# Kernel optimization log

Measured on AMD Instinct MI355X. Metric: run time of the kernel, lower is better.

## Reference

```python
import jax, jax.numpy as jnp
import numpy as np

N, E, G = 50000, 800000, 256
H, C = 8, 16
F0 = 64
FH = H * C  # 128
L = 6
EPS = 1e-5
SEL = [0, 1, 2, 3, 4, 5, 5, 5]  # <10 layers -> pad with last


def setup_inputs() -> dict:
    key = jax.random.key(0)
    ks = jax.random.split(key, 32)

    def w(k, shape, fan_in):
        return jax.random.normal(k, shape, jnp.float32) / np.float32(np.sqrt(fan_in))

    inp = {
        'x': jax.random.normal(ks[0], (N, F0), jnp.float32),
        'edge_index': jax.random.randint(ks[1], (2, E), 0, N),
        'batch_vec': jnp.sort(jax.random.randint(ks[2], (N,), 0, G)),
        # layer 0 (in=F0)
        'Wq0': w(ks[3], (F0, FH), F0), 'bq0': 0.01 * jax.random.normal(ks[4], (FH,), jnp.float32),
        'Wk0': w(ks[5], (F0, FH), F0), 'bk0': 0.01 * jax.random.normal(ks[6], (FH,), jnp.float32),
        'Wv0': w(ks[7], (F0, FH), F0), 'bv0': 0.01 * jax.random.normal(ks[8], (FH,), jnp.float32),
        'Ws0': w(ks[9], (F0, FH), F0), 'bs0': 0.01 * jax.random.normal(ks[10], (FH,), jnp.float32),
        # layers 1..L-1 (in=FH), stacked
        'Wq': w(ks[11], (L - 1, FH, FH), FH), 'bq': 0.01 * jax.random.normal(ks[12], (L - 1, FH), jnp.float32),
        'Wk': w(ks[13], (L - 1, FH, FH), FH), 'bk': 0.01 * jax.random.normal(ks[14], (L - 1, FH), jnp.float32),
        'Wv': w(ks[15], (L - 1, FH, FH), FH), 'bv': 0.01 * jax.random.normal(ks[16], (L - 1, FH), jnp.float32),
        'Ws': w(ks[17], (L - 1, FH, FH), FH), 'bs': 0.01 * jax.random.normal(ks[18], (L - 1, FH), jnp.float32),
        # BatchNorm affine params per layer
        'gamma': jnp.ones((L, FH), jnp.float32),
        'beta': jnp.zeros((L, FH), jnp.float32),
    }
    return inp


def _transformer_conv(x, src, dst, Wq, bq, Wk, bk, Wv, bv, Ws, bs):
    # q from target nodes, k/v from source nodes (PyG TransformerConv, concat=True)
    q = (x @ Wq + bq).reshape(-1, H, C)
    k = (x @ Wk + bk).reshape(-1, H, C)
    v = (x @ Wv + bv).reshape(-1, H, C)
    s = jnp.einsum('ehc,ehc->eh', q[dst], k[src]) * np.float32(1.0 / np.sqrt(C))  # [E,H]
    m = jax.ops.segment_max(s, dst, num_segments=N)       # segment softmax over in-edges
    e = jnp.exp(s - m[dst])
    denom = jax.ops.segment_sum(e, dst, num_segments=N)
    alpha = e / jnp.maximum(denom[dst], 1e-16)            # [E,H]
    msg = jax.ops.segment_sum(alpha[:, :, None] * v[src], dst, num_segments=N)  # [N,H,C]
    return msg.reshape(-1, FH) + (x @ Ws + bs)            # root/skip connection


def _bn_relu(x, g, b):
    mu = jnp.mean(x, axis=0)
    var = jnp.var(x, axis=0)  # biased, as used for normalization in training mode
    return jax.nn.relu((x - mu) * jax.lax.rsqrt(var + EPS) * g + b)


def reference(x, edge_index, batch_vec, Wq0, bq0, Wk0, bk0, Wv0, bv0, Ws0, bs0,
              Wq, bq, Wk, bk, Wv, bv, Ws, bs, gamma, beta):
    src, dst = edge_index[0], edge_index[1]
    outs = []
    h = _bn_relu(_transformer_conv(x, src, dst, Wq0, bq0, Wk0, bk0, Wv0, bv0, Ws0, bs0),
                 gamma[0], beta[0])
    outs.append(h)
    for i in range(L - 1):
        h = _bn_relu(_transformer_conv(h, src, dst, Wq[i], bq[i], Wk[i], bk[i],
                                       Wv[i], bv[i], Ws[i], bs[i]),
                     gamma[i + 1], beta[i + 1])
        outs.append(h)
    counts = jnp.maximum(jax.ops.segment_sum(jnp.ones((N,), x.dtype), batch_vec, num_segments=G), 1.0)
    pooled = [jax.ops.segment_sum(o, batch_vec, num_segments=G) / counts[:, None] for o in outs]
    latent = jnp.stack([pooled[i] for i in SEL], axis=1)  # [G, 8, FH]
    return latent.reshape(G, -1)                          # [G, 8*FH]
```

## Files before the change

kernel.cpp:

```cpp
#include <hip/hip_runtime.h>
#include <hip/hip_bf16.h>
#include <math.h>

#define NN 50000
#define NE 800000
#define NG 256
#define FHH 128
#define NL 6
#define NCH 49
#define NB 391

typedef __attribute__((ext_vector_type(8))) short s16x8;
typedef __attribute__((ext_vector_type(4))) float f32x4;

#define QSCALE 0.36067376022224085f

#if defined(__has_builtin)
#if __has_builtin(__builtin_amdgcn_fdot2_f32_bf16)
#define HAVE_BFDOT 1
#endif
#endif
#ifndef HAVE_BFDOT
#define HAVE_BFDOT 0
#endif

__device__ __forceinline__ ushort f2bf(float x) {
  uint u = __float_as_uint(x);
  u += 0x7fffu + ((u >> 16) & 1u);
  return (ushort)(u >> 16);
}
__device__ __forceinline__ float bf2f(ushort h) {
  return __uint_as_float(((uint)h) << 16);
}
__device__ __forceinline__ float bfl(uint u) { return __uint_as_float(u << 16); }
__device__ __forceinline__ float bfh(uint u) { return __uint_as_float(u & 0xffff0000u); }
__device__ __forceinline__ uint packbf(float a, float b) {
  return (uint)f2bf(a) | ((uint)f2bf(b) << 16);
}

#if HAVE_BFDOT
typedef __attribute__((ext_vector_type(2))) __bf16 bf16v2;
__device__ __forceinline__ float dot2acc(uint a, uint b, float acc) {
  return __builtin_amdgcn_fdot2_f32_bf16(__builtin_bit_cast(bf16v2, a),
                                         __builtin_bit_cast(bf16v2, b), acc, false);
}
#endif

__device__ __forceinline__ void gload16(const ushort* g, ushort* l) {
  __builtin_amdgcn_global_load_lds(
      (const __attribute__((address_space(1))) uint*)(const void*)g,
      (__attribute__((address_space(3))) uint*)(void*)l, 16, 0, 0);
}

__global__ void k_gstart(const int* __restrict__ bv, int* __restrict__ gstart) {
  int g = blockIdx.x * blockDim.x + threadIdx.x;
  if (g > NG) return;
  int lo = 0, hi = NN;
  while (lo < hi) { int mid = (lo + hi) >> 1; if (bv[mid] < g) lo = mid + 1; else hi = mid; }
  gstart[g] = lo;
}

__global__ void k_deg(const int* __restrict__ dstv, int* __restrict__ deg) {
  int e = blockIdx.x * blockDim.x + threadIdx.x;
  if (e < NE) atomicAdd(&deg[dstv[e]], 1);
}

__global__ __launch_bounds__(256) void k_scanA(const int* __restrict__ deg, int* __restrict__ part) {
  int b = blockIdx.x, t = threadIdx.x;
  int s = 0;
  for (int j = t; j < 1024; j += 256) { int i = b * 1024 + j; if (i < NN) s += deg[i]; }
  __shared__ int sh[4];
  for (int o = 32; o; o >>= 1) s += __shfl_down(s, o, 64);
  if ((t & 63) == 0) sh[t >> 6] = s;
  __syncthreads();
  if (t == 0) part[b] = sh[0] + sh[1] + sh[2] + sh[3];
}

__global__ void k_scanB(int* __restrict__ part, int* __restrict__ row_ptr) {
  if (threadIdx.x == 0 && blockIdx.x == 0) {
    int run = 0;
    for (int i = 0; i < NCH; ++i) { int v = part[i]; part[i] = run; run += v; }
    row_ptr[NN] = run;
  }
}

__global__ __launch_bounds__(1024) void k_scanC(const int* __restrict__ deg, const int* __restrict__ part,
                                                int* __restrict__ row_ptr, int* __restrict__ cursor) {
  __shared__ int buf[1024];
  int b = blockIdx.x, t = threadIdx.x;
  int i = b * 1024 + t;
  int v = (i < NN) ? deg[i] : 0;
  buf[t] = v;
  __syncthreads();
  for (int off = 1; off < 1024; off <<= 1) {
    int add = (t >= off) ? buf[t - off] : 0;
    __syncthreads();
    buf[t] += add;
    __syncthreads();
  }
  if (i < NN) { int ex = part[b] + buf[t] - v; row_ptr[i] = ex; cursor[i] = ex; }
}

__global__ void k_scatter(const int* __restrict__ srcv, const int* __restrict__ dstv,
                          int* __restrict__ cursor, uint* __restrict__ colb) {
  int e = blockIdx.x * blockDim.x + threadIdx.x;
  if (e < NE) {
    int d = dstv[e];
    int pos = atomicAdd(&cursor[d], 1);
    colb[pos] = ((uint)srcv[e]) << 9;
  }
}

__device__ __forceinline__ size_t wtile_idx(int k, int c) {
  return (size_t)(k >> 5) * 4096 + ((((c >> 4) * 4 + ((k & 31) >> 3)) * 16 + (c & 15)) * 8 + (k & 7));
}

__global__ __launch_bounds__(256) void k_wconv0(const float* __restrict__ W0, const float* __restrict__ W1,
                                                const float* __restrict__ W2, const float* __restrict__ W3,
                                                ushort* __restrict__ wh, ushort* __restrict__ wl) {
  int id = blockIdx.x * 256 + threadIdx.x;
  if (id >= 4 * 64 * 128) return;
  int mat = id >> 13, rem = id & 8191;
  int k = rem >> 7, c = rem & 127;
  const float* W = (mat == 0) ? W0 : (mat == 1) ? W1 : (mat == 2) ? W2 : W3;
  float v = W[k * 128 + c];
  ushort h = f2bf(v);
  ushort lo = f2bf(v - bf2f(h));
  size_t dst = (size_t)mat * 8192 + wtile_idx(k, c);
  wh[dst] = h; wl[dst] = lo;
}

__global__ __launch_bounds__(256) void k_wconvS(const float* __restrict__ Wq, const float* __restrict__ Wk,
                                                const float* __restrict__ Wv, const float* __restrict__ Ws,
                                                ushort* __restrict__ wh, ushort* __restrict__ wl) {
  int id = blockIdx.x * 256 + threadIdx.x;
  if (id >= 5 * 4 * 16384) return;
  int lay = id / 65536, rem = id % 65536;
  int mat = rem >> 14, rem2 = rem & 16383;
  int k = rem2 >> 7, c = rem2 & 127;
  const float* W = (mat == 0) ? Wq : (mat == 1) ? Wk : (mat == 2) ? Wv : Ws;
  float v = W[(size_t)lay * 16384 + k * 128 + c];
  ushort h = f2bf(v);
  ushort lo = f2bf(v - bf2f(h));
  size_t dst = 32768 + ((size_t)lay * 4 + mat) * 16384 + wtile_idx(k, c);
  wh[dst] = h; wl[dst] = lo;
}

template <int K>
__global__ __launch_bounds__(256) void k_presplit(const float* __restrict__ Y,
                                                  ushort* __restrict__ Xh) {
  const int CP = K / 4;
  int idx = blockIdx.x * 256 + threadIdx.x;
  int row = idx / CP;
  int c4 = (idx % CP) * 4;
  if (row >= NN) return;
  float4 v = *reinterpret_cast<const float4*>(Y + (size_t)row * K + c4);
  ushort h0 = f2bf(v.x), h1 = f2bf(v.y), h2 = f2bf(v.z), h3 = f2bf(v.w);
  int b = row >> 7, g = (row & 127) >> 4, frow = row & 15;
  int ks = c4 >> 5, qq = (c4 & 31) >> 3, j = c4 & 7;
  size_t base = ((size_t)ks * NB + b) * 4096 + (((g * 4 + qq) * 16) + frow) * 8 + j;
  *reinterpret_cast<uint2*>(Xh + base) =
      make_uint2((uint)h0 | ((uint)h1 << 16), (uint)h2 | ((uint)h3 << 16));
}

template <int K>
__global__ __launch_bounds__(256, 3) void k_gemm(
    const ushort* __restrict__ Xh,
    const ushort* __restrict__ Wth, const ushort* __restrict__ Wtl,
    const float* __restrict__ b0, const float* __restrict__ b1,
    const float* __restrict__ b2, const float* __restrict__ b3,
    ushort* __restrict__ qbf, ushort* __restrict__ kv, ushort* __restrict__ xsb) {
  __shared__ __align__(16) ushort Ah[4096];
  __shared__ __align__(16) ushort Bh[4096];
  __shared__ __align__(16) ushort Bl[4096];
  int bid = blockIdx.x;
  int mat = (bid >> 3) & 3;
  int b = (bid & 7) + ((bid >> 5) << 3);
  if (b >= NB) return;
  int t = threadIdx.x;
  int lane = t & 63, w = t >> 6;
  int wr = w >> 1, wc = w & 1;
  int frow = lane & 15;
  const ushort* wh = Wth + (size_t)mat * (K * 128);
  const ushort* wl = Wtl + (size_t)mat * (K * 128);
  const float* bb = (mat == 0) ? b0 : (mat == 1) ? b1 : (mat == 2) ? b2 : b3;

  f32x4 acc[4][4];
#pragma unroll
  for (int i = 0; i < 4; ++i)
#pragma unroll
    for (int j = 0; j < 4; ++j)
#pragma unroll
      for (int r = 0; r < 4; ++r) acc[i][j][r] = 0.f;

  int wofs = w * 1024 + lane * 8;
  for (int ks = 0; ks < K / 32; ++ks) {
    size_t abase = ((size_t)ks * NB + b) * 4096;
    const ushort* gAh = Xh + abase + wofs;
    const ushort* gBh = wh + ks * 4096 + wofs;
    const ushort* gBl = wl + ks * 4096 + wofs;
    gload16(gAh, &Ah[w * 1024]);
    gload16(gAh + 512, &Ah[w * 1024 + 512]);
    gload16(gBh, &Bh[w * 1024]);
    gload16(gBh + 512, &Bh[w * 1024 + 512]);
    gload16(gBl, &Bl[w * 1024]);
    gload16(gBl + 512, &Bl[w * 1024 + 512]);
    __syncthreads();
    s16x8 ah[4], bh[4], bl[4];
#pragma unroll
    for (int g = 0; g < 4; ++g) {
      ah[g] = *reinterpret_cast<const s16x8*>(&Ah[(wr * 4 + g) * 512 + lane * 8]);
      bh[g] = *reinterpret_cast<const s16x8*>(&Bh[(wc * 4 + g) * 512 + lane * 8]);
      bl[g] = *reinterpret_cast<const s16x8*>(&Bl[(wc * 4 + g) * 512 + lane * 8]);
    }
#pragma unroll
    for (int rg = 0; rg < 4; ++rg)
#pragma unroll
      for (int cg = 0; cg < 4; ++cg) {
        acc[rg][cg] = __builtin_amdgcn_mfma_f32_16x16x32_bf16(ah[rg], bh[cg], acc[rg][cg], 0, 0, 0);
        acc[rg][cg] = __builtin_amdgcn_mfma_f32_16x16x32_bf16(ah[rg], bl[cg], acc[rg][cg], 0, 0, 0);
      }
    __syncthreads();
  }
  int r0 = b * 128;
  int qq = (lane >> 4) << 2;
#pragma unroll
  for (int rg = 0; rg < 4; ++rg) {
#pragma unroll
    for (int cg = 0; cg < 4; ++cg) {
      int colg = wc * 64 + cg * 16 + frow;
      float bv = bb[colg];
#pragma unroll
      for (int r = 0; r < 4; ++r) {
        int row = r0 + wr * 64 + rg * 16 + qq + r;
        if (row >= NN) continue;
        float val = acc[rg][cg][r] + bv;
        if (mat == 0)      qbf[(size_t)row * FHH + colg] = f2bf(val * QSCALE);
        else if (mat == 3) xsb[(size_t)row * FHH + colg] = f2bf(val);
        else {
          int pos = (colg >> 1) * 4 + ((mat == 2) ? 2 : 0) + (colg & 1);
          kv[(size_t)row * 256 + pos] = f2bf(val);
        }
      }
    }
  }
}

__global__ __launch_bounds__(256) void k_agg(const uint* __restrict__ qb,
                                             const ushort* __restrict__ kv,
                                             const uint* __restrict__ xsb,
                                             const int* __restrict__ row_ptr,
                                             const uint* __restrict__ colb,
                                             uint* __restrict__ yb) {
  int n = blockIdx.x * 4 + (threadIdx.x >> 6);
  int lane = threadIdx.x & 63;
  int hl = lane & 31, half = lane >> 5;
  uint2 qp = *reinterpret_cast<const uint2*>(qb + (n << 6) + 2 * hl);
#if !HAVE_BFDOT
  float qa = bfl(qp.x), qbv = bfh(qp.x), qc = bfl(qp.y), qd = bfh(qp.y);
#endif
  const char* kvb = (const char*)kv;
  uint tof = (uint)hl * 16u;
  int e0 = row_ptr[n], e1 = row_ptr[n + 1];
  float sum = 0.f, a0 = 0.f, a1 = 0.f, a2 = 0.f, a3 = 0.f;
  int i = e0;
#define QKDOT(d, p)                                                    \
  {                                                                    \
    p = qa * bfl(d.x);                                                 \
    p = fmaf(qbv, bfh(d.x), p);                                        \
    p = fmaf(qc, bfl(d.z), p);                                         \
    p = fmaf(qd, bfh(d.z), p);                                         \
  }
  for (; i + 8 <= e1; i += 8) {
    uint oA = colb[i + half] + tof;
    uint oB = colb[i + 2 + half] + tof;
    uint oC = colb[i + 4 + half] + tof;
    uint oD = colb[i + 6 + half] + tof;
    uint4 dA = *(const uint4*)(kvb + oA);
    uint4 dB = *(const uint4*)(kvb + oB);
    uint4 dC = *(const uint4*)(kvb + oC);
    uint4 dD = *(const uint4*)(kvb + oD);
    float pA, pB, pC, pD;
#if HAVE_BFDOT
    pA = dot2acc(dA.z, qp.y, dot2acc(dA.x, qp.x, 0.f));
    pB = dot2acc(dB.z, qp.y, dot2acc(dB.x, qp.x, 0.f));
    pC = dot2acc(dC.z, qp.y, dot2acc(dC.x, qp.x, 0.f));
    pD = dot2acc(dD.z, qp.y, dot2acc(dD.x, qp.x, 0.f));
#else
    QKDOT(dA, pA) QKDOT(dB, pB) QKDOT(dC, pC) QKDOT(dD, pD)
#endif
    pA += __shfl_xor(pA, 1, 4);  pB += __shfl_xor(pB, 1, 4);
    pC += __shfl_xor(pC, 1, 4);  pD += __shfl_xor(pD, 1, 4);
    pA += __shfl_xor(pA, 2, 4);  pB += __shfl_xor(pB, 2, 4);
    pC += __shfl_xor(pC, 2, 4);  pD += __shfl_xor(pD, 2, 4);
    float wA = exp2f(fminf(pA, 110.f));
    float wB = exp2f(fminf(pB, 110.f));
    float wC = exp2f(fminf(pC, 110.f));
    float wD = exp2f(fminf(pD, 110.f));
    sum += (wA + wB) + (wC + wD);
    a0 = fmaf(wA, bfl(dA.y), fmaf(wB, bfl(dB.y), fmaf(wC, bfl(dC.y), fmaf(wD, bfl(dD.y), a0))));
    a1 = fmaf(wA, bfh(dA.y), fmaf(wB, bfh(dB.y), fmaf(wC, bfh(dC.y), fmaf(wD, bfh(dD.y), a1))));
    a2 = fmaf(wA, bfl(dA.w), fmaf(wB, bfl(dB.w), fmaf(wC, bfl(dC.w), fmaf(wD, bfl(dD.w), a2))));
    a3 = fmaf(wA, bfh(dA.w), fmaf(wB, bfh(dB.w), fmaf(wC, bfh(dC.w), fmaf(wD, bfh(dD.w), a3))));
  }
  for (; i + 2 <= e1; i += 2) {
    uint oA = colb[i + half] + tof;
    uint4 dA = *(const uint4*)(kvb + oA);
    float pA;
#if HAVE_BFDOT
    pA = dot2acc(dA.z, qp.y, dot2acc(dA.x, qp.x, 0.f));
#else
    QKDOT(dA, pA)
#endif
    pA += __shfl_xor(pA, 1, 4);
    pA += __shfl_xor(pA, 2, 4);
    float wA = exp2f(fminf(pA, 110.f));
    sum += wA;
    a0 = fmaf(wA, bfl(dA.y), a0);
    a1 = fmaf(wA, bfh(dA.y), a1);
    a2 = fmaf(wA, bfl(dA.w), a2);
    a3 = fmaf(wA, bfh(dA.w), a3);
  }
  if (i < e1) {
    uint oA = colb[i] + tof;
    uint4 dA = *(const uint4*)(kvb + oA);
    float pA;
#if HAVE_BFDOT
    pA = dot2acc(dA.z, qp.y, dot2acc(dA.x, qp.x, 0.f));
#else
    QKDOT(dA, pA)
#endif
    pA += __shfl_xor(pA, 1, 4);
    pA += __shfl_xor(pA, 2, 4);
    float wA = exp2f(fminf(pA, 110.f));
    if (half) wA = 0.f;
    sum += wA;
    a0 = fmaf(wA, bfl(dA.y), a0);
    a1 = fmaf(wA, bfh(dA.y), a1);
    a2 = fmaf(wA, bfl(dA.w), a2);
    a3 = fmaf(wA, bfh(dA.w), a3);
  }
#undef QKDOT
  sum += __shfl_xor(sum, 32);
  a0 += __shfl_xor(a0, 32);
  a1 += __shfl_xor(a1, 32);
  a2 += __shfl_xor(a2, 32);
  a3 += __shfl_xor(a3, 32);
  float inv = 1.f / fmaxf(sum, 1e-16f);
  uint2 xv = *reinterpret_cast<const uint2*>(xsb + (n << 6) + 2 * hl);
  float o0 = fmaf(a0, inv, bfl(xv.x));
  float o1 = fmaf(a1, inv, bfh(xv.x));
  float o2 = fmaf(a2, inv, bfl(xv.y));
  float o3 = fmaf(a3, inv, bfh(xv.y));
  if (half == 0) {
    uint2 o;
    o.x = packbf(o0, o1);
    o.y = packbf(o2, o3);
    *reinterpret_cast<uint2*>(yb + (n << 6) + 2 * hl) = o;
  }
}

__global__ __launch_bounds__(256) void k_bnstats(const uint* __restrict__ yb,
                                                 float* __restrict__ stats) {
  __shared__ float2 s1[256], s2[256];
  int u = threadIdx.x & 63;
  int grp = threadIdx.x >> 6;
  float2 a = make_float2(0.f, 0.f), b = make_float2(0.f, 0.f);
  for (int r = blockIdx.x * 4 + grp; r < NN; r += 1024) {
    uint d = yb[(size_t)r * 64 + u];
    float x = bfl(d), yv = bfh(d);
    a.x += x; a.y += yv;
    b.x = fmaf(x, x, b.x); b.y = fmaf(yv, yv, b.y);
  }
  s1[threadIdx.x] = a;
  s2[threadIdx.x] = b;
  __syncthreads();
  if (grp == 0) {
#pragma unroll
    for (int g = 1; g < 4; ++g) {
      a.x += s1[u + 64 * g].x; a.y += s1[u + 64 * g].y;
      b.x += s2[u + 64 * g].x; b.y += s2[u + 64 * g].y;
    }
    atomicAdd(&stats[2 * u], a.x);
    atomicAdd(&stats[2 * u + 1], a.y);
    atomicAdd(&stats[128 + 2 * u], b.x);
    atomicAdd(&stats[128 + 2 * u + 1], b.y);
  }
}

template <int WRITE_X>
__global__ __launch_bounds__(256) void k_post(const uint* __restrict__ yb,
                                              const float* __restrict__ st,
                                              const float* __restrict__ gvec,
                                              const float* __restrict__ bvec_,
                                              const int* __restrict__ bv,
                                              const int* __restrict__ gstart,
                                              float* __restrict__ out, int layer,
                                              ushort* __restrict__ Xh) {
  __shared__ float acts[8][128];
  __shared__ int sg[8];
  __shared__ float ssc[128], ssh[128];
  int b = blockIdx.x, t = threadIdx.x;
  if (t < 128) {
    const float invn = 1.f / (float)NN;
    float mu = st[t] * invn;
    float var = st[128 + t] * invn - mu * mu;
    float sc = gvec[t] * rsqrtf(var + 1e-5f);
    ssc[t] = sc;
    ssh[t] = bvec_[t] - mu * sc;
  }
  if (t < 8) sg[t] = (b * 8 + t < NN) ? bv[b * 8 + t] : -1;
  __syncthreads();
  int row = b * 8 + (t >> 5);
  int c4 = (t & 31) * 4;
  bool ok = row < NN;
  float4 a = make_float4(0.f, 0.f, 0.f, 0.f);
  if (ok) {
    uint2 u2 = *reinterpret_cast<const uint2*>(yb + (size_t)row * 64 + (c4 >> 1));
    a.x = fmaxf(fmaf(bfl(u2.x), ssc[c4 + 0], ssh[c4 + 0]), 0.f);
    a.y = fmaxf(fmaf(bfh(u2.x), ssc[c4 + 1], ssh[c4 + 1]), 0.f);
    a.z = fmaxf(fmaf(bfl(u2.y), ssc[c4 + 2], ssh[c4 + 2]), 0.f);
    a.w = fmaxf(fmaf(bfh(u2.y), ssc[c4 + 3], ssh[c4 + 3]), 0.f);
  }
  *reinterpret_cast<float4*>(&acts[t >> 5][c4]) = a;
  if (WRITE_X && ok) {
    ushort h0 = f2bf(a.x), h1 = f2bf(a.y), h2 = f2bf(a.z), h3 = f2bf(a.w);
    int bb = row >> 7, g = (row & 127) >> 4, frow = row & 15;
    int ks = c4 >> 5, qq = (c4 & 31) >> 3, j = c4 & 7;
    size_t base = ((size_t)ks * NB + bb) * 4096 + (((g * 4 + qq) * 16) + frow) * 8 + j;
    *reinterpret_cast<uint2*>(Xh + base) =
        make_uint2((uint)h0 | ((uint)h1 << 16), (uint)h2 | ((uint)h3 << 16));
  }
  __syncthreads();
  if (t < 128) {
    float racc = 0.f;
    int cg = sg[0];
    for (int r = 0; r < 8; ++r) {
      int g = sg[r];
      if (g != cg) {
        if (cg >= 0) {
          float p = racc / (float)(gstart[cg + 1] - gstart[cg]);
          if (layer < 5) atomicAdd(&out[(size_t)cg * 1024 + layer * FHH + t], p);
          else {
            atomicAdd(&out[(size_t)cg * 1024 + 5 * FHH + t], p);
            atomicAdd(&out[(size_t)cg * 1024 + 6 * FHH + t], p);
            atomicAdd(&out[(size_t)cg * 1024 + 7 * FHH + t], p);
          }
        }
        racc = 0.f;
        cg = g;
      }
      racc += acts[r][t];
    }
    if (cg >= 0) {
      float p = racc / (float)(gstart[cg + 1] - gstart[cg]);
      if (layer < 5) atomicAdd(&out[(size_t)cg * 1024 + layer * FHH + t], p);
      else {
        atomicAdd(&out[(size_t)cg * 1024 + 5 * FHH + t], p);
        atomicAdd(&out[(size_t)cg * 1024 + 6 * FHH + t], p);
        atomicAdd(&out[(size_t)cg * 1024 + 7 * FHH + t], p);
      }
    }
  }
}

extern "C" void kernel_launch(void* const* d_in, const int* in_sizes, int n_in,
                              void* d_out, int out_size, void* d_ws, size_t ws_size,
                              hipStream_t stream) {
  (void)in_sizes; (void)n_in; (void)ws_size;
  const float* x    = (const float*)d_in[0];
  const int*   ei   = (const int*)d_in[1];
  const int*   bvec = (const int*)d_in[2];
  const float* Wq0  = (const float*)d_in[3];
  const float* bq0  = (const float*)d_in[4];
  const float* Wk0  = (const float*)d_in[5];
  const float* bk0  = (const float*)d_in[6];
  const float* Wv0  = (const float*)d_in[7];
  const float* bv0  = (const float*)d_in[8];
  const float* Ws0  = (const float*)d_in[9];
  const float* bs0  = (const float*)d_in[10];
  const float* WqS  = (const float*)d_in[11];
  const float* bqS  = (const float*)d_in[12];
  const float* WkS  = (const float*)d_in[13];
  const float* bkS  = (const float*)d_in[14];
  const float* WvS  = (const float*)d_in[15];
  const float* bvS  = (const float*)d_in[16];
  const float* WsS  = (const float*)d_in[17];
  const float* bsS  = (const float*)d_in[18];
  const float* gamma = (const float*)d_in[19];
  const float* beta  = (const float*)d_in[20];
  float* out = (float*)d_out;

  char* ws = (char*)d_ws;
  size_t off = 0;
  auto alloc = [&](size_t bytes) {
    void* p = ws + off;
    off = (off + bytes + 255) & ~(size_t)255;
    return p;
  };
  ushort* qbf = (ushort*)alloc((size_t)NN * FHH * 2);
  ushort* xsb = (ushort*)alloc((size_t)NN * FHH * 2);
  uint* yb    = (uint*)alloc((size_t)NN * 64 * 4);
  ushort* kv  = (ushort*)alloc((size_t)NN * 256 * 2);
  ushort* Xh  = (ushort*)alloc((size_t)4 * NB * 4096 * 2 + 8192);
  uint* colb   = (uint*)alloc((size_t)NE * 4);
  int* row_ptr = (int*)alloc((size_t)(NN + 1) * 4);
  int* cursor  = (int*)alloc((size_t)NN * 4);
  int* deg     = (int*)alloc((size_t)NN * 4);
  int* part    = (int*)alloc((size_t)NCH * 4);
  int* gstart  = (int*)alloc((size_t)(NG + 1) * 4);
  float* bstat = (float*)alloc((size_t)NL * 2 * FHH * 4);
  ushort* wsh = (ushort*)alloc((size_t)360448 * 2);
  ushort* wsl = (ushort*)alloc((size_t)360448 * 2);

  const int* srcv = ei;
  const int* dstv = ei + NE;

  hipMemsetAsync(out, 0, (size_t)out_size * 4, stream);
  hipMemsetAsync(deg, 0, (size_t)NN * 4, stream);
  hipMemsetAsync(bstat, 0, (size_t)NL * 2 * FHH * 4, stream);
  k_gstart<<<5, 64, 0, stream>>>(bvec, gstart);
  k_deg<<<(NE + 255) / 256, 256, 0, stream>>>(dstv, deg);
  k_scanA<<<NCH, 256, 0, stream>>>(deg, part);
  k_scanB<<<1, 64, 0, stream>>>(part, row_ptr);
  k_scanC<<<NCH, 1024, 0, stream>>>(deg, part, row_ptr, cursor);
  k_scatter<<<(NE + 255) / 256, 256, 0, stream>>>(srcv, dstv, cursor, colb);
  k_wconv0<<<128, 256, 0, stream>>>(Wq0, Wk0, Wv0, Ws0, wsh, wsl);
  k_wconvS<<<1280, 256, 0, stream>>>(WqS, WkS, WvS, WsS, wsh, wsl);
  k_presplit<64><<<(NN * 16 + 255) / 256, 256, 0, stream>>>(x, Xh);

  const int GEMM_GRID = 49 * 32;
  for (int l = 0; l < NL; ++l) {
    const ushort* WthL = wsh + ((l == 0) ? 0 : (size_t)32768 + (size_t)(l - 1) * 65536);
    const ushort* WtlL = wsl + ((l == 0) ? 0 : (size_t)32768 + (size_t)(l - 1) * 65536);
    const float *bq_, *bk_, *bv_, *bs_;
    if (l == 0) { bq_ = bq0; bk_ = bk0; bv_ = bv0; bs_ = bs0; }
    else {
      size_t bo = (size_t)(l - 1) * FHH;
      bq_ = bqS + bo; bk_ = bkS + bo; bv_ = bvS + bo; bs_ = bsS + bo;
    }
    if (l == 0)
      k_gemm<64><<<GEMM_GRID, 256, 0, stream>>>(Xh, WthL, WtlL, bq_, bk_, bv_, bs_, qbf, kv, xsb);
    else
      k_gemm<128><<<GEMM_GRID, 256, 0, stream>>>(Xh, WthL, WtlL, bq_, bk_, bv_, bs_, qbf, kv, xsb);
    k_agg<<<NN / 4, 256, 0, stream>>>((const uint*)qbf, kv, (const uint*)xsb, row_ptr, colb, yb);
    float* lstat = bstat + (size_t)l * 2 * FHH;
    k_bnstats<<<256, 256, 0, stream>>>(yb, lstat);
    if (l + 1 < NL)
      k_post<1><<<6250, 256, 0, stream>>>(yb, lstat, gamma + (size_t)l * FHH,
                                          beta + (size_t)l * FHH, bvec, gstart, out, l, Xh);
    else
      k_post<0><<<6250, 256, 0, stream>>>(yb, lstat, gamma + (size_t)l * FHH,
                                          beta + (size_t)l * FHH, bvec, gstart, out, l, Xh);
  }
}
```

Baseline: 901.3 us.

## Fuse all layer kernels into one persistent cooperative kernel with grid syncs

Replaces the 24 per-layer launches (gemm, agg, bnstats, post) with a single cooperative persistent kernel that loops over layers and phases, separated by grid-wide syncs. Blocks walk tiles and nodes with grid-stride loops, sized from the occupancy query. The aim is to remove launch overhead and inter-kernel gaps. The cost is grid.sync overhead, lower occupancy from one shared register and LDS budget across all phases, and loss of the bf16 dot2 path in the aggregation.

```diff
diff --git a/kernel.cpp b/kernel.cpp
--- a/kernel.cpp
+++ b/kernel.cpp
@@ -1,6 +1,9 @@
 #include <hip/hip_runtime.h>
 #include <hip/hip_bf16.h>
+#include <hip/hip_cooperative_groups.h>
 #include <math.h>
+
+namespace cg = cooperative_groups;
 
 #define NN 50000
 #define NE 800000
@@ -9,20 +12,12 @@
 #define NL 6
 #define NCH 49
 #define NB 391
+#define NTILE (49 * 32)
 
 typedef __attribute__((ext_vector_type(8))) short s16x8;
 typedef __attribute__((ext_vector_type(4))) float f32x4;
 
 #define QSCALE 0.36067376022224085f
-
-#if defined(__has_builtin)
-#if __has_builtin(__builtin_amdgcn_fdot2_f32_bf16)
-#define HAVE_BFDOT 1
-#endif
-#endif
-#ifndef HAVE_BFDOT
-#define HAVE_BFDOT 0
-#endif
 
 __device__ __forceinline__ ushort f2bf(float x) {
   uint u = __float_as_uint(x);
@@ -37,14 +32,6 @@
 __device__ __forceinline__ uint packbf(float a, float b) {
   return (uint)f2bf(a) | ((uint)f2bf(b) << 16);
 }
-
-#if HAVE_BFDOT
-typedef __attribute__((ext_vector_type(2))) __bf16 bf16v2;
-__device__ __forceinline__ float dot2acc(uint a, uint b, float acc) {
-  return __builtin_amdgcn_fdot2_f32_bf16(__builtin_bit_cast(bf16v2, a),
-                                         __builtin_bit_cast(bf16v2, b), acc, false);
-}
-#endif
 
 __device__ __forceinline__ void gload16(const ushort* g, ushort* l) {
   __builtin_amdgcn_global_load_lds(
@@ -163,304 +150,316 @@
       make_uint2((uint)h0 | ((uint)h1 << 16), (uint)h2 | ((uint)h3 << 16));
 }
 
-template <int K>
-__global__ __launch_bounds__(256, 3) void k_gemm(
-    const ushort* __restrict__ Xh,
-    const ushort* __restrict__ Wth, const ushort* __restrict__ Wtl,
-    const float* __restrict__ b0, const float* __restrict__ b1,
-    const float* __restrict__ b2, const float* __restrict__ b3,
-    ushort* __restrict__ qbf, ushort* __restrict__ kv, ushort* __restrict__ xsb) {
-  __shared__ __align__(16) ushort Ah[4096];
-  __shared__ __align__(16) ushort Bh[4096];
-  __shared__ __align__(16) ushort Bl[4096];
-  int bid = blockIdx.x;
-  int mat = (bid >> 3) & 3;
-  int b = (bid & 7) + ((bid >> 5) << 3);
-  if (b >= NB) return;
-  int t = threadIdx.x;
-  int lane = t & 63, w = t >> 6;
-  int wr = w >> 1, wc = w & 1;
-  int frow = lane & 15;
-  const ushort* wh = Wth + (size_t)mat * (K * 128);
-  const ushort* wl = Wtl + (size_t)mat * (K * 128);
-  const float* bb = (mat == 0) ? b0 : (mat == 1) ? b1 : (mat == 2) ? b2 : b3;
-
-  f32x4 acc[4][4];
-#pragma unroll
-  for (int i = 0; i < 4; ++i)
-#pragma unroll
-    for (int j = 0; j < 4; ++j)
-#pragma unroll
-      for (int r = 0; r < 4; ++r) acc[i][j][r] = 0.f;
-
-  int wofs = w * 1024 + lane * 8;
-  for (int ks = 0; ks < K / 32; ++ks) {
-    size_t abase = ((size_t)ks * NB + b) * 4096;
-    const ushort* gAh = Xh + abase + wofs;
-    const ushort* gBh = wh + ks * 4096 + wofs;
-    const ushort* gBl = wl + ks * 4096 + wofs;
-    gload16(gAh, &Ah[w * 1024]);
-    gload16(gAh + 512, &Ah[w * 1024 + 512]);
-    gload16(gBh, &Bh[w * 1024]);
-    gload16(gBh + 512, &Bh[w * 1024 + 512]);
-    gload16(gBl, &Bl[w * 1024]);
-    gload16(gBl + 512, &Bl[w * 1024 + 512]);
-    __syncthreads();
-    s16x8 ah[4], bh[4], bl[4];
-#pragma unroll
-    for (int g = 0; g < 4; ++g) {
-      ah[g] = *reinterpret_cast<const s16x8*>(&Ah[(wr * 4 + g) * 512 + lane * 8]);
-      bh[g] = *reinterpret_cast<const s16x8*>(&Bh[(wc * 4 + g) * 512 + lane * 8]);
-      bl[g] = *reinterpret_cast<const s16x8*>(&Bl[(wc * 4 + g) * 512 + lane * 8]);
+__global__ __launch_bounds__(256) void k_layers(
+    const ushort* __restrict__ wsh, const ushort* __restrict__ wsl,
+    const float* __restrict__ bq0, const float* __restrict__ bk0,
+    const float* __restrict__ bv0, const float* __restrict__ bs0,
+    const float* __restrict__ bqS, const float* __restrict__ bkS,
+    const float* __restrict__ bvS, const float* __restrict__ bsS,
+    const float* __restrict__ gamma, const float* __restrict__ beta,
+    const int* __restrict__ bvec, const int* __restrict__ gstart,
+    const int* __restrict__ row_ptr, const uint* __restrict__ colb,
+    ushort* __restrict__ qbf, ushort* __restrict__ kv, ushort* __restrict__ xsb,
+    uint* __restrict__ yb, ushort* __restrict__ Xh,
+    float* __restrict__ bstat, float* __restrict__ out) {
+  cg::grid_group grid = cg::this_grid();
+  __shared__ __align__(16) char sbuf[24576];
+  ushort* Ah = (ushort*)sbuf;
+  ushort* Bh = (ushort*)(sbuf + 8192);
+  ushort* Bl = (ushort*)(sbuf + 16384);
+  const int NBLK = gridDim.x;
+  const int t = threadIdx.x;
+
+  for (int l = 0; l < NL; ++l) {
+    const int K = (l == 0) ? 64 : 128;
+    const int nks = K >> 5;
+    const int matstride = K << 7;
+    const ushort* WthL = wsh + ((l == 0) ? 0 : (size_t)32768 + (size_t)(l - 1) * 65536);
+    const ushort* WtlL = wsl + ((l == 0) ? 0 : (size_t)32768 + (size_t)(l - 1) * 65536);
+    const float *bq_, *bk_, *bv_, *bs_;
+    if (l == 0) { bq_ = bq0; bk_ = bk0; bv_ = bv0; bs_ = bs0; }
+    else {
+      size_t bo = (size_t)(l - 1) * FHH;
+      bq_ = bqS + bo; bk_ = bkS + bo; bv_ = bvS + bo; bs_ = bsS + bo;
     }
-#pragma unroll
-    for (int rg = 0; rg < 4; ++rg)
-#pragma unroll
-      for (int cg = 0; cg < 4; ++cg) {
-        acc[rg][cg] = __builtin_amdgcn_mfma_f32_16x16x32_bf16(ah[rg], bh[cg], acc[rg][cg], 0, 0, 0);
-        acc[rg][cg] = __builtin_amdgcn_mfma_f32_16x16x32_bf16(ah[rg], bl[cg], acc[rg][cg], 0, 0, 0);
-      }
-    __syncthreads();
-  }
-  int r0 = b * 128;
-  int qq = (lane >> 4) << 2;
-#pragma unroll
-  for (int rg = 0; rg < 4; ++rg) {
-#pragma unroll
-    for (int cg = 0; cg < 4; ++cg) {
-      int colg = wc * 64 + cg * 16 + frow;
-      float bv = bb[colg];
-#pragma unroll
-      for (int r = 0; r < 4; ++r) {
-        int row = r0 + wr * 64 + rg * 16 + qq + r;
-        if (row >= NN) continue;
-        float val = acc[rg][cg][r] + bv;
-        if (mat == 0)      qbf[(size_t)row * FHH + colg] = f2bf(val * QSCALE);
-        else if (mat == 3) xsb[(size_t)row * FHH + colg] = f2bf(val);
-        else {
-          int pos = (colg >> 1) * 4 + ((mat == 2) ? 2 : 0) + (colg & 1);
-          kv[(size_t)row * 256 + pos] = f2bf(val);
-        }
+    float* lstat = bstat + (size_t)l * 2 * FHH;
+
+    {
+      int lane = t & 63, w = t >> 6;
+      int wr = w >> 1, wc = w & 1;
+      int frow = lane & 15;
+      int wofs = w * 1024 + lane * 8;
+      for (int tile = blockIdx.x; tile < NTILE; tile += NBLK) {
+        int mat = (tile >> 3) & 3;
+        int b = (tile & 7) + ((tile >> 5) << 3);
+        if (b < NB) {
+          const ushort* wh = WthL + (size_t)mat * matstride;
+          const ushort* wl = WtlL + (size_t)mat * matstride;
+          const float* bb = (mat == 0) ? bq_ : (mat == 1) ? bk_ : (mat == 2) ? bv_ : bs_;
+          f32x4 acc[4][4];
+#pragma unroll
+          for (int i = 0; i < 4; ++i)
+#pragma unroll
+            for (int j = 0; j < 4; ++j)
+#pragma unroll
+              for (int r = 0; r < 4; ++r) acc[i][j][r] = 0.f;
+          for (int ks = 0; ks < nks; ++ks) {
+            size_t abase = ((size_t)ks * NB + b) * 4096;
+            const ushort* gAh = Xh + abase + wofs;
+            const ushort* gBh = wh + ks * 4096 + wofs;
+            const ushort* gBl = wl + ks * 4096 + wofs;
+            gload16(gAh, &Ah[w * 1024]);
+            gload16(gAh + 512, &Ah[w * 1024 + 512]);
+            gload16(gBh, &Bh[w * 1024]);
+            gload16(gBh + 512, &Bh[w * 1024 + 512]);
+            gload16(gBl, &Bl[w * 1024]);
+            gload16(gBl + 512, &Bl[w * 1024 + 512]);
+            __syncthreads();
+            s16x8 ah[4], bh[4], bl[4];
+#pragma unroll
+            for (int g = 0; g < 4; ++g) {
+              ah[g] = *reinterpret_cast<const s16x8*>(&Ah[(wr * 4 + g) * 512 + lane * 8]);
+              bh[g] = *reinterpret_cast<const s16x8*>(&Bh[(wc * 4 + g) * 512 + lane * 8]);
+              bl[g] = *reinterpret_cast<const s16x8*>(&Bl[(wc * 4 + g) * 512 + lane * 8]);
+            }
+#pragma unroll
+            for (int rg = 0; rg < 4; ++rg)
+#pragma unroll
+              for (int cg2 = 0; cg2 < 4; ++cg2) {
+                acc[rg][cg2] = __builtin_amdgcn_mfma_f32_16x16x32_bf16(ah[rg], bh[cg2], acc[rg][cg2], 0, 0, 0);
+                acc[rg][cg2] = __builtin_amdgcn_mfma_f32_16x16x32_bf16(ah[rg], bl[cg2], acc[rg][cg2], 0, 0, 0);
+              }
+            __syncthreads();
+          }
+          int r0 = b * 128;
+          int qq = (lane >> 4) << 2;
+#pragma unroll
+          for (int rg = 0; rg < 4; ++rg) {
+#pragma unroll
+            for (int cg2 = 0; cg2 < 4; ++cg2) {
+              int colg = wc * 64 + cg2 * 16 + frow;
+              float bv = bb[colg];
+#pragma unroll
+              for (int r = 0; r < 4; ++r) {
+                int row = r0 + wr * 64 + rg * 16 + qq + r;
+                if (row >= NN) continue;
+                float val = acc[rg][cg2][r] + bv;
+                if (mat == 0)      qbf[(size_t)row * FHH + colg] = f2bf(val * QSCALE);
+                else if (mat == 3) xsb[(size_t)row * FHH + colg] = f2bf(val);
+                else {
+                  int pos = (colg >> 1) * 4 + ((mat == 2) ? 2 : 0) + (colg & 1);
+                  kv[(size_t)row * 256 + pos] = f2bf(val);
+                }
+              }
+            }
+          }
+        }
+        __syncthreads();
       }
     }
-  }
-}
-
-__global__ __launch_bounds__(256) void k_agg(const uint* __restrict__ qb,
-                                             const ushort* __restrict__ kv,
-                                             const uint* __restrict__ xsb,
-                                             const int* __restrict__ row_ptr,
-                                             const uint* __restrict__ colb,
-                                             uint* __restrict__ yb) {
-  int n = blockIdx.x * 4 + (threadIdx.x >> 6);
-  int lane = threadIdx.x & 63;
-  int hl = lane & 31, half = lane >> 5;
-  uint2 qp = *reinterpret_cast<const uint2*>(qb + (n << 6) + 2 * hl);
-#if !HAVE_BFDOT
-  float qa = bfl(qp.x), qbv = bfh(qp.x), qc = bfl(qp.y), qd = bfh(qp.y);
-#endif
-  const char* kvb = (const char*)kv;
-  uint tof = (uint)hl * 16u;
-  int e0 = row_ptr[n], e1 = row_ptr[n + 1];
-  float sum = 0.f, a0 = 0.f, a1 = 0.f, a2 = 0.f, a3 = 0.f;
-  int i = e0;
-#define QKDOT(d, p)                                                    \
-  {                                                                    \
-    p = qa * bfl(d.x);                                                 \
-    p = fmaf(qbv, bfh(d.x), p);                                        \
-    p = fmaf(qc, bfl(d.z), p);                                         \
-    p = fmaf(qd, bfh(d.z), p);                                         \
-  }
-  for (; i + 8 <= e1; i += 8) {
-    uint oA = colb[i + half] + tof;
-    uint oB = colb[i + 2 + half] + tof;
-    uint oC = colb[i + 4 + half] + tof;
-    uint oD = colb[i + 6 + half] + tof;
-    uint4 dA = *(const uint4*)(kvb + oA);
-    uint4 dB = *(const uint4*)(kvb + oB);
-    uint4 dC = *(const uint4*)(kvb + oC);
-    uint4 dD = *(const uint4*)(kvb + oD);
-    float pA, pB, pC, pD;
-#if HAVE_BFDOT
-    pA = dot2acc(dA.z, qp.y, dot2acc(dA.x, qp.x, 0.f));
-    pB = dot2acc(dB.z, qp.y, dot2acc(dB.x, qp.x, 0.f));
-    pC = dot2acc(dC.z, qp.y, dot2acc(dC.x, qp.x, 0.f));
-    pD = dot2acc(dD.z, qp.y, dot2acc(dD.x, qp.x, 0.f));
-#else
-    QKDOT(dA, pA) QKDOT(dB, pB) QKDOT(dC, pC) QKDOT(dD, pD)
-#endif
-    pA += __shfl_xor(pA, 1, 4);  pB += __shfl_xor(pB, 1, 4);
-    pC += __shfl_xor(pC, 1, 4);  pD += __shfl_xor(pD, 1, 4);
-    pA += __shfl_xor(pA, 2, 4);  pB += __shfl_xor(pB, 2, 4);
-    pC += __shfl_xor(pC, 2, 4);  pD += __shfl_xor(pD, 2, 4);
-    float wA = exp2f(fminf(pA, 110.f));
-    float wB = exp2f(fminf(pB, 110.f));
-    float wC = exp2f(fminf(pC, 110.f));
-    float wD = exp2f(fminf(pD, 110.f));
-    sum += (wA + wB) + (wC + wD);
-    a0 = fmaf(wA, bfl(dA.y), fmaf(wB, bfl(dB.y), fmaf(wC, bfl(dC.y), fmaf(wD, bfl(dD.y), a0))));
-    a1 = fmaf(wA, bfh(dA.y), fmaf(wB, bfh(dB.y), fmaf(wC, bfh(dC.y), fmaf(wD, bfh(dD.y), a1))));
-    a2 = fmaf(wA, bfl(dA.w), fmaf(wB, bfl(dB.w), fmaf(wC, bfl(dC.w), fmaf(wD, bfl(dD.w), a2))));
-    a3 = fmaf(wA, bfh(dA.w), fmaf(wB, bfh(dB.w), fmaf(wC, bfh(dC.w), fmaf(wD, bfh(dD.w), a3))));
-  }
-  for (; i + 2 <= e1; i += 2) {
-    uint oA = colb[i + half] + tof;
-    uint4 dA = *(const uint4*)(kvb + oA);
-    float pA;
-#if HAVE_BFDOT
-    pA = dot2acc(dA.z, qp.y, dot2acc(dA.x, qp.x, 0.f));
-#else
-    QKDOT(dA, pA)
-#endif
-    pA += __shfl_xor(pA, 1, 4);
-    pA += __shfl_xor(pA, 2, 4);
-    float wA = exp2f(fminf(pA, 110.f));
-    sum += wA;
-    a0 = fmaf(wA, bfl(dA.y), a0);
-    a1 = fmaf(wA, bfh(dA.y), a1);
-    a2 = fmaf(wA, bfl(dA.w), a2);
-    a3 = fmaf(wA, bfh(dA.w), a3);
-  }
-  if (i < e1) {
-    uint oA = colb[i] + tof;
-    uint4 dA = *(const uint4*)(kvb + oA);
-    float pA;
-#if HAVE_BFDOT
-    pA = dot2acc(dA.z, qp.y, dot2acc(dA.x, qp.x, 0.f));
-#else
-    QKDOT(dA, pA)
-#endif
-    pA += __shfl_xor(pA, 1, 4);
-    pA += __shfl_xor(pA, 2, 4);
-    float wA = exp2f(fminf(pA, 110.f));
-    if (half) wA = 0.f;
-    sum += wA;
-    a0 = fmaf(wA, bfl(dA.y), a0);
-    a1 = fmaf(wA, bfh(dA.y), a1);
-    a2 = fmaf(wA, bfl(dA.w), a2);
-    a3 = fmaf(wA, bfh(dA.w), a3);
-  }
+    grid.sync();
+
+    {
+      const uint* qb = (const uint*)qbf;
+      const uint* xsu = (const uint*)xsb;
+      const char* kvb = (const char*)kv;
+      int lane = t & 63;
+      int hl = lane & 31, half = lane >> 5;
+      uint tof = (uint)hl * 16u;
+      for (int nb = blockIdx.x; nb < NN / 4; nb += NBLK) {
+        int n = nb * 4 + (t >> 6);
+        uint2 qp = *reinterpret_cast<const uint2*>(qb + (n << 6) + 2 * hl);
+        float qa = bfl(qp.x), qbv = bfh(qp.x), qc = bfl(qp.y), qd = bfh(qp.y);
+        int e0 = row_ptr[n], e1 = row_ptr[n + 1];
+        float sum = 0.f, a0 = 0.f, a1 = 0.f, a2 = 0.f, a3 = 0.f;
+        int i = e0;
+#define QKDOT(d, p)                                                  \
+        {                                                            \
+          p = qa * bfl(d.x);                                         \
+          p = fmaf(qbv, bfh(d.x), p);                                \
+          p = fmaf(qc, bfl(d.z), p);                                 \
+          p = fmaf(qd, bfh(d.z), p);                                 \
+        }
+        for (; i + 8 <= e1; i += 8) {
+          uint oA = colb[i + half] + tof;
+          uint oB = colb[i + 2 + half] + tof;
+          uint oC = colb[i + 4 + half] + tof;
+          uint oD = colb[i + 6 + half] + tof;
+          uint4 dA = *(const uint4*)(kvb + oA);
+          uint4 dB = *(const uint4*)(kvb + oB);
+          uint4 dC = *(const uint4*)(kvb + oC);
+          uint4 dD = *(const uint4*)(kvb + oD);
+          float pA, pB, pC, pD;
+          QKDOT(dA, pA) QKDOT(dB, pB) QKDOT(dC, pC) QKDOT(dD, pD)
+          pA += __shfl_xor(pA, 1, 4);  pB += __shfl_xor(pB, 1, 4);
+          pC += __shfl_xor(pC, 1, 4);  pD += __shfl_xor(pD, 1, 4);
+          pA += __shfl_xor(pA, 2, 4);  pB += __shfl_xor(pB, 2, 4);
+          pC += __shfl_xor(pC, 2, 4);  pD += __shfl_xor(pD, 2, 4);
+          float wA = exp2f(fminf(pA, 110.f));
+          float wB = exp2f(fminf(pB, 110.f));
+          float wC = exp2f(fminf(pC, 110.f));
+          float wD = exp2f(fminf(pD, 110.f));
+          sum += (wA + wB) + (wC + wD);
+          a0 = fmaf(wA, bfl(dA.y), fmaf(wB, bfl(dB.y), fmaf(wC, bfl(dC.y), fmaf(wD, bfl(dD.y), a0))));
+          a1 = fmaf(wA, bfh(dA.y), fmaf(wB, bfh(dB.y), fmaf(wC, bfh(dC.y), fmaf(wD, bfh(dD.y), a1))));
+          a2 = fmaf(wA, bfl(dA.w), fmaf(wB, bfl(dB.w), fmaf(wC, bfl(dC.w), fmaf(wD, bfl(dD.w), a2))));
+          a3 = fmaf(wA, bfh(dA.w), fmaf(wB, bfh(dB.w), fmaf(wC, bfh(dC.w), fmaf(wD, bfh(dD.w), a3))));
+        }
+        for (; i + 2 <= e1; i += 2) {
+          uint oA = colb[i + half] + tof;
+          uint4 dA = *(const uint4*)(kvb + oA);
+          float pA;
+          QKDOT(dA, pA)
+          pA += __shfl_xor(pA, 1, 4);
+          pA += __shfl_xor(pA, 2, 4);
+          float wA = exp2f(fminf(pA, 110.f));
+          sum += wA;
+          a0 = fmaf(wA, bfl(dA.y), a0);
+          a1 = fmaf(wA, bfh(dA.y), a1);
+          a2 = fmaf(wA, bfl(dA.w), a2);
+          a3 = fmaf(wA, bfh(dA.w), a3);
+        }
+        if (i < e1) {
+          uint oA = colb[i] + tof;
+          uint4 dA = *(const uint4*)(kvb + oA);
+          float pA;
+          QKDOT(dA, pA)
+          pA += __shfl_xor(pA, 1, 4);
+          pA += __shfl_xor(pA, 2, 4);
+          float wA = exp2f(fminf(pA, 110.f));
+          if (half) wA = 0.f;
+          sum += wA;
+          a0 = fmaf(wA, bfl(dA.y), a0);
+          a1 = fmaf(wA, bfh(dA.y), a1);
+          a2 = fmaf(wA, bfl(dA.w), a2);
+          a3 = fmaf(wA, bfh(dA.w), a3);
+        }
 #undef QKDOT
-  sum += __shfl_xor(sum, 32);
-  a0 += __shfl_xor(a0, 32);
-  a1 += __shfl_xor(a1, 32);
-  a2 += __shfl_xor(a2, 32);
-  a3 += __shfl_xor(a3, 32);
-  float inv = 1.f / fmaxf(sum, 1e-16f);
-  uint2 xv = *reinterpret_cast<const uint2*>(xsb + (n << 6) + 2 * hl);
-  float o0 = fmaf(a0, inv, bfl(xv.x));
-  float o1 = fmaf(a1, inv, bfh(xv.x));
-  float o2 = fmaf(a2, inv, bfl(xv.y));
-  float o3 = fmaf(a3, inv, bfh(xv.y));
-  if (half == 0) {
-    uint2 o;
-    o.x = packbf(o0, o1);
-    o.y = packbf(o2, o3);
-    *reinterpret_cast<uint2*>(yb + (n << 6) + 2 * hl) = o;
-  }
-}
-
-__global__ __launch_bounds__(256) void k_bnstats(const uint* __restrict__ yb,
-                                                 float* __restrict__ stats) {
-  __shared__ float2 s1[256], s2[256];
-  int u = threadIdx.x & 63;
-  int grp = threadIdx.x >> 6;
-  float2 a = make_float2(0.f, 0.f), b = make_float2(0.f, 0.f);
-  for (int r = blockIdx.x * 4 + grp; r < NN; r += 1024) {
-    uint d = yb[(size_t)r * 64 + u];
-    float x = bfl(d), yv = bfh(d);
-    a.x += x; a.y += yv;
-    b.x = fmaf(x, x, b.x); b.y = fmaf(yv, yv, b.y);
-  }
-  s1[threadIdx.x] = a;
-  s2[threadIdx.x] = b;
-  __syncthreads();
-  if (grp == 0) {
-#pragma unroll
-    for (int g = 1; g < 4; ++g) {
-      a.x += s1[u + 64 * g].x; a.y += s1[u + 64 * g].y;
-      b.x += s2[u + 64 * g].x; b.y += s2[u + 64 * g].y;
-    }
-    atomicAdd(&stats[2 * u], a.x);
-    atomicAdd(&stats[2 * u + 1], a.y);
-    atomicAdd(&stats[128 + 2 * u], b.x);
-    atomicAdd(&stats[128 + 2 * u + 1], b.y);
-  }
-}
-
-template <int WRITE_X>
-__global__ __launch_bounds__(256) void k_post(const uint* __restrict__ yb,
-                                              const float* __restrict__ st,
-                                              const float* __restrict__ gvec,
-                                              const float* __restrict__ bvec_,
-                                              const int* __restrict__ bv,
-                                              const int* __restrict__ gstart,
-                                              float* __restrict__ out, int layer,
-                                              ushort* __restrict__ Xh) {
-  __shared__ float acts[8][128];
-  __shared__ int sg[8];
-  __shared__ float ssc[128], ssh[128];
-  int b = blockIdx.x, t = threadIdx.x;
-  if (t < 128) {
-    const float invn = 1.f / (float)NN;
-    float mu = st[t] * invn;
-    float var = st[128 + t] * invn - mu * mu;
-    float sc = gvec[t] * rsqrtf(var + 1e-5f);
-    ssc[t] = sc;
-    ssh[t] = bvec_[t] - mu * sc;
-  }
-  if (t < 8) sg[t] = (b * 8 + t < NN) ? bv[b * 8 + t] : -1;
-  __syncthreads();
-  int row = b * 8 + (t >> 5);
-  int c4 = (t & 31) * 4;
-  bool ok = row < NN;
-  float4 a = make_float4(0.f, 0.f, 0.f, 0.f);
-  if (ok) {
-    uint2 u2 = *reinterpret_cast<const uint2*>(yb + (size_t)row * 64 + (c4 >> 1));
-    a.x = fmaxf(fmaf(bfl(u2.x), ssc[c4 + 0], ssh[c4 + 0]), 0.f);
-    a.y = fmaxf(fmaf(bfh(u2.x), ssc[c4 + 1], ssh[c4 + 1]), 0.f);
-    a.z = fmaxf(fmaf(bfl(u2.y), ssc[c4 + 2], ssh[c4 + 2]), 0.f);
-    a.w = fmaxf(fmaf(bfh(u2.y), ssc[c4 + 3], ssh[c4 + 3]), 0.f);
-  }
-  *reinterpret_cast<float4*>(&acts[t >> 5][c4]) = a;
-  if (WRITE_X && ok) {
-    ushort h0 = f2bf(a.x), h1 = f2bf(a.y), h2 = f2bf(a.z), h3 = f2bf(a.w);
-    int bb = row >> 7, g = (row & 127) >> 4, frow = row & 15;
-    int ks = c4 >> 5, qq = (c4 & 31) >> 3, j = c4 & 7;
-    size_t base = ((size_t)ks * NB + bb) * 4096 + (((g * 4 + qq) * 16) + frow) * 8 + j;
-    *reinterpret_cast<uint2*>(Xh + base) =
-        make_uint2((uint)h0 | ((uint)h1 << 16), (uint)h2 | ((uint)h3 << 16));
-  }
-  __syncthreads();
-  if (t < 128) {
-    float racc = 0.f;
-    int cg = sg[0];
-    for (int r = 0; r < 8; ++r) {
-      int g = sg[r];
-      if (g != cg) {
-        if (cg >= 0) {
-          float p = racc / (float)(gstart[cg + 1] - gstart[cg]);
-          if (layer < 5) atomicAdd(&out[(size_t)cg * 1024 + layer * FHH + t], p);
-          else {
-            atomicAdd(&out[(size_t)cg * 1024 + 5 * FHH + t], p);
-            atomicAdd(&out[(size_t)cg * 1024 + 6 * FHH + t], p);
-            atomicAdd(&out[(size_t)cg * 1024 + 7 * FHH + t], p);
-          }
-        }
-        racc = 0.f;
-        cg = g;
-      }
-      racc += acts[r][t];
-    }
-    if (cg >= 0) {
-      float p = racc / (float)(gstart[cg + 1] - gstart[cg]);
-      if (layer < 5) atomicAdd(&out[(size_t)cg * 1024 + layer * FHH + t], p);
-      else {
-        atomicAdd(&out[(size_t)cg * 1024 + 5 * FHH + t], p);
-        atomicAdd(&out[(size_t)cg * 1024 + 6 * FHH + t], p);
-        atomicAdd(&out[(size_t)cg * 1024 + 7 * FHH + t], p);
+        sum += __shfl_xor(sum, 32);
+        a0 += __shfl_xor(a0, 32);
+        a1 += __shfl_xor(a1, 32);
+        a2 += __shfl_xor(a2, 32);
+        a3 += __shfl_xor(a3, 32);
+        float inv = 1.f / fmaxf(sum, 1e-16f);
+        uint2 xv = *reinterpret_cast<const uint2*>(xsu + (n << 6) + 2 * hl);
+        float o0 = fmaf(a0, inv, bfl(xv.x));
+        float o1 = fmaf(a1, inv, bfh(xv.x));
+        float o2 = fmaf(a2, inv, bfl(xv.y));
+        float o3 = fmaf(a3, inv, bfh(xv.y));
+        if (half == 0) {
+          uint2 o;
+          o.x = packbf(o0, o1);
+          o.y = packbf(o2, o3);
+          *reinterpret_cast<uint2*>(yb + (n << 6) + 2 * hl) = o;
+        }
       }
     }
+    grid.sync();
+
+    {
+      float2* s1 = (float2*)sbuf;
+      float2* s2 = (float2*)(sbuf + 2048);
+      int u = t & 63;
+      int grp = t >> 6;
+      float2 a = make_float2(0.f, 0.f), b2 = make_float2(0.f, 0.f);
+      for (int r = blockIdx.x * 4 + grp; r < NN; r += NBLK * 4) {
+        uint d = yb[(size_t)r * 64 + u];
+        float x = bfl(d), yv = bfh(d);
+        a.x += x; a.y += yv;
+        b2.x = fmaf(x, x, b2.x); b2.y = fmaf(yv, yv, b2.y);
+      }
+      s1[t] = a;
+      s2[t] = b2;
+      __syncthreads();
+      if (grp == 0) {
+#pragma unroll
+        for (int g = 1; g < 4; ++g) {
+          a.x += s1[u + 64 * g].x; a.y += s1[u + 64 * g].y;
+          b2.x += s2[u + 64 * g].x; b2.y += s2[u + 64 * g].y;
+        }
+        atomicAdd(&lstat[2 * u], a.x);
+        atomicAdd(&lstat[2 * u + 1], a.y);
+        atomicAdd(&lstat[128 + 2 * u], b2.x);
+        atomicAdd(&lstat[128 + 2 * u + 1], b2.y);
+      }
+      __syncthreads();
+    }
+    grid.sync();
+
+    {
+      float (*acts)[128] = (float(*)[128])sbuf;
+      int* sg = (int*)(sbuf + 4096);
+      float* ssc = (float*)(sbuf + 4352);
+      float* ssh = (float*)(sbuf + 4864);
+      const float* gvec = gamma + (size_t)l * FHH;
+      const float* bvec_ = beta + (size_t)l * FHH;
+      int write_x = (l + 1 < NL);
+      for (int pb = blockIdx.x; pb < 6250; pb += NBLK) {
+        if (t < 128) {
+          const float invn = 1.f / (float)NN;
+          float mu = lstat[t] * invn;
+          float var = lstat[128 + t] * invn - mu * mu;
+          float sc = gvec[t] * rsqrtf(var + 1e-5f);
+          ssc[t] = sc;
+          ssh[t] = bvec_[t] - mu * sc;
+        }
+        if (t < 8) sg[t] = (pb * 8 + t < NN) ? bvec[pb * 8 + t] : -1;
+        __syncthreads();
+        int row = pb * 8 + (t >> 5);
+        int c4 = (t & 31) * 4;
+        bool ok = row < NN;
+        float4 a = make_float4(0.f, 0.f, 0.f, 0.f);
+        if (ok) {
+          uint2 u2 = *reinterpret_cast<const uint2*>(yb + (size_t)row * 64 + (c4 >> 1));
+          a.x = fmaxf(fmaf(bfl(u2.x), ssc[c4 + 0], ssh[c4 + 0]), 0.f);
+          a.y = fmaxf(fmaf(bfh(u2.x), ssc[c4 + 1], ssh[c4 + 1]), 0.f);
+          a.z = fmaxf(fmaf(bfl(u2.y), ssc[c4 + 2], ssh[c4 + 2]), 0.f);
+          a.w = fmaxf(fmaf(bfh(u2.y), ssc[c4 + 3], ssh[c4 + 3]), 0.f);
+        }
+        *reinterpret_cast<float4*>(&acts[t >> 5][c4]) = a;
+        if (write_x && ok) {
+          ushort h0 = f2bf(a.x), h1 = f2bf(a.y), h2 = f2bf(a.z), h3 = f2bf(a.w);
+          int bb2 = row >> 7, g = (row & 127) >> 4, frow = row & 15;
+          int ks = c4 >> 5, qq = (c4 & 31) >> 3, j = c4 & 7;
+          size_t base = ((size_t)ks * NB + bb2) * 4096 + (((g * 4 + qq) * 16) + frow) * 8 + j;
+          *reinterpret_cast<uint2*>(Xh + base) =
+              make_uint2((uint)h0 | ((uint)h1 << 16), (uint)h2 | ((uint)h3 << 16));
+        }
+        __syncthreads();
+        if (t < 128) {
+          float racc = 0.f;
+          int cgp = sg[0];
+          for (int r = 0; r < 8; ++r) {
+            int g = sg[r];
+            if (g != cgp) {
+              if (cgp >= 0) {
+                float p = racc / (float)(gstart[cgp + 1] - gstart[cgp]);
+                if (l < 5) atomicAdd(&out[(size_t)cgp * 1024 + l * FHH + t], p);
+                else {
+                  atomicAdd(&out[(size_t)cgp * 1024 + 5 * FHH + t], p);
+                  atomicAdd(&out[(size_t)cgp * 1024 + 6 * FHH + t], p);
+                  atomicAdd(&out[(size_t)cgp * 1024 + 7 * FHH + t], p);
+                }
+              }
+              racc = 0.f;
+              cgp = g;
+            }
+            racc += acts[r][t];
+          }
+          if (cgp >= 0) {
+            float p = racc / (float)(gstart[cgp + 1] - gstart[cgp]);
+            if (l < 5) atomicAdd(&out[(size_t)cgp * 1024 + l * FHH + t], p);
+            else {
+              atomicAdd(&out[(size_t)cgp * 1024 + 5 * FHH + t], p);
+              atomicAdd(&out[(size_t)cgp * 1024 + 6 * FHH + t], p);
+              atomicAdd(&out[(size_t)cgp * 1024 + 7 * FHH + t], p);
+            }
+          }
+        }
+        __syncthreads();
+      }
+    }
+    grid.sync();
   }
 }
 
@@ -529,28 +528,22 @@
   k_wconvS<<<1280, 256, 0, stream>>>(WqS, WkS, WvS, WsS, wsh, wsl);
   k_presplit<64><<<(NN * 16 + 255) / 256, 256, 0, stream>>>(x, Xh);
 
-  const int GEMM_GRID = 49 * 32;
-  for (int l = 0; l < NL; ++l) {
-    const ushort* WthL = wsh + ((l == 0) ? 0 : (size_t)32768 + (size_t)(l - 1) * 65536);
-    const ushort* WtlL = wsl + ((l == 0) ? 0 : (size_t)32768 + (size_t)(l - 1) * 65536);
-    const float *bq_, *bk_, *bv_, *bs_;
-    if (l == 0) { bq_ = bq0; bk_ = bk0; bv_ = bv0; bs_ = bs0; }
-    else {
-      size_t bo = (size_t)(l - 1) * FHH;
-      bq_ = bqS + bo; bk_ = bkS + bo; bv_ = bvS + bo; bs_ = bsS + bo;
-    }
-    if (l == 0)
-      k_gemm<64><<<GEMM_GRID, 256, 0, stream>>>(Xh, WthL, WtlL, bq_, bk_, bv_, bs_, qbf, kv, xsb);
-    else
-      k_gemm<128><<<GEMM_GRID, 256, 0, stream>>>(Xh, WthL, WtlL, bq_, bk_, bv_, bs_, qbf, kv, xsb);
-    k_agg<<<NN / 4, 256, 0, stream>>>((const uint*)qbf, kv, (const uint*)xsb, row_ptr, colb, yb);
-    float* lstat = bstat + (size_t)l * 2 * FHH;
-    k_bnstats<<<256, 256, 0, stream>>>(yb, lstat);
-    if (l + 1 < NL)
-      k_post<1><<<6250, 256, 0, stream>>>(yb, lstat, gamma + (size_t)l * FHH,
-                                          beta + (size_t)l * FHH, bvec, gstart, out, l, Xh);
-    else
-      k_post<0><<<6250, 256, 0, stream>>>(yb, lstat, gamma + (size_t)l * FHH,
-                                          beta + (size_t)l * FHH, bvec, gstart, out, l, Xh);
-  }
-}
+  int maxB = 0;
+  hipOccupancyMaxActiveBlocksPerMultiprocessor(&maxB, k_layers, 256, 0);
+  if (maxB < 1) maxB = 1;
+  long nblk = (long)maxB * 256;
+  if (nblk > 3136) nblk = 3136;
+  const ushort* wsh_c = wsh;
+  const ushort* wsl_c = wsl;
+  void* kargs[] = {
+    (void*)&wsh_c, (void*)&wsl_c,
+    (void*)&bq0, (void*)&bk0, (void*)&bv0, (void*)&bs0,
+    (void*)&bqS, (void*)&bkS, (void*)&bvS, (void*)&bsS,
+    (void*)&gamma, (void*)&beta,
+    (void*)&bvec, (void*)&gstart, (void*)&row_ptr, (void*)&colb,
+    (void*)&qbf, (void*)&kv, (void*)&xsb, (void*)&yb, (void*)&Xh,
+    (void*)&bstat, (void*)&out
+  };
+  hipLaunchCooperativeKernel((void*)k_layers, dim3((uint)nblk), dim3(256),
+                             kargs, 0, stream);
+}
```

Measured after the change: 2.534 ms. 181% more time.
